# Kernel optimization log

Hardware: AMD Instinct MI355X
Metric: run time of the kernel (lower is better)

The kernel has to match this reference:

```python
import jax, jax.numpy as jnp
import numpy as np

B, S, IN, OUT, E, K = 4, 2048, 4096, 4096, 8, 16
POOLS = E * K  # 128 rank-one pools


def setup_inputs() -> dict:
    key = jax.random.key(0)
    k1, k2, k3, k4, k5 = jax.random.split(key, 5)
    sc = 0.02
    return {
        "hidden_states": jax.random.normal(k1, (B, S, IN), jnp.float32),
        "w0": jax.random.normal(k2, (OUT, IN), jnp.float32) * sc,   # pretrained Linear weight
        "b0": jnp.zeros((OUT,), jnp.float32),                        # pretrained Linear bias
        "wr": jax.random.normal(k3, (POOLS, IN), jnp.float32) * sc,  # Router stacked v.T
        "u": jax.random.normal(k4, (OUT, POOLS), jnp.float32) * sc,  # RankOnePools.u
        "svh": jax.random.normal(k5, (POOLS, IN), jnp.float32) * sc, # RankOnePools.svh
        "top_k": 2,
    }


def reference(hidden_states, w0, b0, wr, u, svh, top_k):
    # pretrained dense path (expert_use_diff=True)
    pretrained_out = jnp.einsum('bsi,oi->bso', hidden_states, w0) + b0

    x = hidden_states.reshape(-1, hidden_states.shape[-1])  # [N, IN]

    # Router: logits over num_experts*k rank-one pools
    logits = jnp.einsum('ni,pi->np', x, wr)                  # [N, POOLS]
    vals, idx = jax.lax.top_k(logits, top_k)                 # [N, top_k]
    vals = vals / jnp.sum(vals, axis=-1, keepdims=True)      # computed but UNUSED (matches original torch code)

    # RankOnePools: gather selected rank-one factors and combine
    svh_sel = svh[idx]                                       # [N, top_k, IN]
    dot = jnp.einsum('ni,nti->nt', x, svh_sel)               # [N, top_k]
    u_sel = u.T[idx]                                         # [N, top_k, OUT]
    expert_out = jnp.einsum('nt,nto->no', dot, u_sel)        # [N, OUT]

    out = pretrained_out + expert_out.reshape(pretrained_out.shape)
    return out
```

## Files before the change

kernel.cpp:

```cpp
#include <hip/hip_runtime.h>

#define K_DIM  4096
#define N_OUT  4096
#define N_TOK  8192
#define N_POOL 128

typedef __bf16 bf16x8 __attribute__((ext_vector_type(8)));
typedef float  f32x4  __attribute__((ext_vector_type(4)));
typedef unsigned short u16x8 __attribute__((ext_vector_type(8)));

#define AS1 __attribute__((address_space(1)))
#define AS3 __attribute__((address_space(3)))

__device__ __forceinline__ unsigned short f2bf(float f) {
    union { float f; unsigned u; } v; v.f = f;
    unsigned r = v.u + 0x7fffu + ((v.u >> 16) & 1u);
    return (unsigned short)(r >> 16);
}
__device__ __forceinline__ float bf2f(unsigned short b) {
    union { unsigned u; float f; } v; v.u = ((unsigned)b) << 16;
    return v.f;
}

__global__ __launch_bounds__(256) void k_convert_w0(const float* __restrict__ w0,
                                                    unsigned short* __restrict__ w0b) {
    size_t base = ((size_t)blockIdx.x * 256 + threadIdx.x) * 8;
    float4 a = *(const float4*)(w0 + base);
    float4 b = *(const float4*)(w0 + base + 4);
    u16x8 r;
    r[0] = f2bf(a.x); r[1] = f2bf(a.y); r[2] = f2bf(a.z); r[3] = f2bf(a.w);
    r[4] = f2bf(b.x); r[5] = f2bf(b.y); r[6] = f2bf(b.z); r[7] = f2bf(b.w);
    *(u16x8*)(w0b + base) = r;
}

__global__ __launch_bounds__(256) void k_convert_x(const float* __restrict__ x,
                                                   unsigned short* __restrict__ xh) {
    size_t base = ((size_t)blockIdx.x * 256 + threadIdx.x) * 8;
    float4 a = *(const float4*)(x + base);
    float4 b = *(const float4*)(x + base + 4);
    u16x8 r;
    r[0] = f2bf(a.x); r[1] = f2bf(a.y); r[2] = f2bf(a.z); r[3] = f2bf(a.w);
    r[4] = f2bf(b.x); r[5] = f2bf(b.y); r[6] = f2bf(b.z); r[7] = f2bf(b.w);
    *(u16x8*)(xh + base) = r;
}

__global__ __launch_bounds__(256) void k_convert_wr(const float* __restrict__ wr,
                                                    unsigned short* __restrict__ wrh) {
    size_t base = ((size_t)blockIdx.x * 256 + threadIdx.x) * 8;
    float4 a = *(const float4*)(wr + base);
    float4 b = *(const float4*)(wr + base + 4);
    u16x8 r;
    r[0] = f2bf(a.x); r[1] = f2bf(a.y); r[2] = f2bf(a.z); r[3] = f2bf(a.w);
    r[4] = f2bf(b.x); r[5] = f2bf(b.y); r[6] = f2bf(b.z); r[7] = f2bf(b.w);
    *(u16x8*)(wrh + base) = r;
}

__global__ __launch_bounds__(256) void k_transpose_u(const float* __restrict__ u,
                                                     float* __restrict__ uT) {
    __shared__ float t[32][65];
    const int o0 = blockIdx.x * 64, p0 = blockIdx.y * 32;
    const int tid = threadIdx.x;
#pragma unroll
    for (int it = 0; it < 8; it++) {
        int o = (tid >> 5) + it * 8;
        t[tid & 31][o] = u[(size_t)(o0 + o) * N_POOL + p0 + (tid & 31)];
    }
    __syncthreads();
#pragma unroll
    for (int it = 0; it < 8; it++) {
        int p = (tid >> 6) + it * 4;
        uT[(size_t)(p0 + p) * N_OUT + o0 + (tid & 63)] = t[p][tid & 63];
    }
}

__global__ __launch_bounds__(256) void k_logits(const unsigned short* __restrict__ xh,
                                                const unsigned short* __restrict__ wrh,
                                                float* __restrict__ lgbuf) {
    const int tid  = threadIdx.x;
    const int lane = tid & 63;
    const int w    = tid >> 6;
    const int lrow = lane & 15, lquad = lane >> 4;
    const size_t tok0 = (size_t)blockIdx.x * 16;
    const int p0 = w * 32;

    const unsigned short* xa  = xh  + (tok0 + lrow) * (size_t)K_DIM + lquad * 8;
    const unsigned short* bp0 = wrh + (size_t)(p0 + lrow) * K_DIM + lquad * 8;
    const unsigned short* bp1 = wrh + (size_t)(p0 + 16 + lrow) * K_DIM + lquad * 8;

    f32x4 acc0 = {}, acc1 = {};
    bf16x8 av = *(const bf16x8*)xa;
    bf16x8 b0 = *(const bf16x8*)bp0;
    bf16x8 b1 = *(const bf16x8*)bp1;

#pragma unroll 4
    for (int s = 0; s < 128; s++) {
        bf16x8 ac = av, b0c = b0, b1c = b1;
        if (s < 127) {
            av = *(const bf16x8*)(xa  + (s + 1) * 32);
            b0 = *(const bf16x8*)(bp0 + (s + 1) * 32);
            b1 = *(const bf16x8*)(bp1 + (s + 1) * 32);
        }
        acc0 = __builtin_amdgcn_mfma_f32_16x16x32_bf16(ac, b0c, acc0, 0, 0, 0);
        acc1 = __builtin_amdgcn_mfma_f32_16x16x32_bf16(ac, b1c, acc1, 0, 0, 0);
    }

#pragma unroll
    for (int r = 0; r < 4; r++) {
        lgbuf[(tok0 + lquad * 4 + r) * N_POOL + p0 + lrow]      = acc0[r];
        lgbuf[(tok0 + lquad * 4 + r) * N_POOL + p0 + 16 + lrow] = acc1[r];
    }
}

#define TAU 0.06f

__global__ __launch_bounds__(256) void k_topk(const float* __restrict__ lgbuf,
                                              const float* __restrict__ x,
                                              const float* __restrict__ wr,
                                              const unsigned short* __restrict__ xh,
                                              const float* __restrict__ svh,
                                              int* __restrict__ idxp,
                                              float* __restrict__ dotp) {
    __shared__ float lg[32][N_POOL + 1];
    __shared__ float thr2[32];
    __shared__ int   flg[32];
    __shared__ int   sel[32][2];

    const int tid  = threadIdx.x;
    const int lane = tid & 63;
    const int w    = tid >> 6;
    const size_t m0 = (size_t)blockIdx.x * 32;

    {
        const int tok = tid >> 3, cb = (tid & 7) * 16;
        const float* src = lgbuf + (m0 + tok) * N_POOL + cb;
#pragma unroll
        for (int j = 0; j < 4; j++) {
            float4 v = *(const float4*)(src + j * 4);
            lg[tok][cb + j * 4 + 0] = v.x; lg[tok][cb + j * 4 + 1] = v.y;
            lg[tok][cb + j * 4 + 2] = v.z; lg[tok][cb + j * 4 + 3] = v.w;
        }
    }
    __syncthreads();

    if (tid < 32) {
        float v1 = -3.4e38f, v2 = -3.4e38f, v3 = -3.4e38f; int i1 = 0, i2 = 0;
        for (int p = 0; p < N_POOL; p++) {
            float v = lg[tid][p];
            if (v > v1)      { v3 = v2; v2 = v1; i2 = i1; v1 = v; i1 = p; }
            else if (v > v2) { v3 = v2; v2 = v;  i2 = p; }
            else if (v > v3) { v3 = v; }
        }
        sel[tid][0] = i1; sel[tid][1] = i2;
        thr2[tid] = v2 - TAU;
        flg[tid]  = (v2 - v3 < TAU) ? 1 : 0;
    }
    __syncthreads();

    if (w == 0) {
        for (int s = 0; s < 32; s++) {
            if (!flg[s]) continue;
            const float th = thr2[s];
            unsigned long long c0 = __ballot(lg[s][lane] >= th);
            unsigned long long c1 = __ballot(lg[s][64 + lane] >= th);
            float v1 = -3.4e38f, v2 = -3.4e38f; int i1 = 0, i2 = 0;
            const float* xr = x + (m0 + s) * K_DIM;
            for (int half = 0; half < 2; half++) {
                unsigned long long m = half ? c1 : c0;
                while (m) {
                    const int p = (half ? 64 : 0) + __ffsll(m) - 1;
                    m &= m - 1;
                    const float* wp = wr + (size_t)p * K_DIM;
                    float d = 0.f;
#pragma unroll 8
                    for (int it = 0; it < 64; it++)
                        d += xr[it * 64 + lane] * wp[it * 64 + lane];
#pragma unroll
                    for (int off = 32; off > 0; off >>= 1) d += __shfl_down(d, off);
                    d = __shfl(d, 0);
                    if (d > v1)      { v2 = v1; i2 = i1; v1 = d; i1 = p; }
                    else if (d > v2) { v2 = d; i2 = p; }
                }
            }
            if (lane == 0) { sel[s][0] = i1; sel[s][1] = i2; }
        }
    }
    __syncthreads();

    if (tid < 32) {
        idxp[(m0 + tid) * 2 + 0] = sel[tid][0];
        idxp[(m0 + tid) * 2 + 1] = sel[tid][1];
    }

    for (int s = w; s < 32; s += 4) {
        const size_t n = m0 + s;
        const int e0 = sel[s][0], e1 = sel[s][1];
        float d0 = 0.f, d1 = 0.f;
#pragma unroll
        for (int it = 0; it < 8; it++) {
            const int e = (it * 64 + lane) * 8;
            u16x8 xv = *(const u16x8*)(xh + n * K_DIM + e);
            float4 s0 = *(const float4*)(svh + (size_t)e0 * K_DIM + e);
            float4 s1 = *(const float4*)(svh + (size_t)e0 * K_DIM + e + 4);
            float4 s2 = *(const float4*)(svh + (size_t)e1 * K_DIM + e);
            float4 s3 = *(const float4*)(svh + (size_t)e1 * K_DIM + e + 4);
            float x0 = bf2f(xv[0]), x1 = bf2f(xv[1]), x2 = bf2f(xv[2]), x3 = bf2f(xv[3]);
            float x4 = bf2f(xv[4]), x5 = bf2f(xv[5]), x6 = bf2f(xv[6]), x7 = bf2f(xv[7]);
            d0 += x0*s0.x + x1*s0.y + x2*s0.z + x3*s0.w + x4*s1.x + x5*s1.y + x6*s1.z + x7*s1.w;
            d1 += x0*s2.x + x1*s2.y + x2*s2.z + x3*s2.w + x4*s3.x + x5*s3.y + x6*s3.z + x7*s3.w;
        }
#pragma unroll
        for (int off = 32; off > 0; off >>= 1) {
            d0 += __shfl_down(d0, off);
            d1 += __shfl_down(d1, off);
        }
        if (lane == 0) { dotp[n * 2 + 0] = d0; dotp[n * 2 + 1] = d1; }
    }
}

__global__ __launch_bounds__(512) void k_gemm(const unsigned short* __restrict__ xh,
                                              const unsigned short* __restrict__ w0b,
                                              const float* __restrict__ b0,
                                              const float* __restrict__ uT,
                                              const int* __restrict__ idxp,
                                              const float* __restrict__ dotp,
                                              float* __restrict__ out) {
    __shared__ __attribute__((aligned(16))) unsigned short Als[2][256 * 64];
    __shared__ __attribute__((aligned(16))) unsigned short Bls[2][256 * 64];

    const int tid  = threadIdx.x;
    const int lane = tid & 63;
    const int w    = tid >> 6;
    const int wm   = w >> 2, wn = w & 3;
    const int lrow = lane & 15, lquad = lane >> 4;

    const int lgid = (blockIdx.x & 7) * 64 + (blockIdx.x >> 3);
    const size_t n0 = (size_t)(lgid & 15) * 256;
    const size_t m0 = (size_t)(lgid >> 4) * 256;

    const int srow   = tid >> 3;
    const int xchunk = (tid & 7) ^ (srow & 7);
    const unsigned short* ag = xh  + (m0 + srow) * K_DIM + xchunk * 8;
    const unsigned short* bg = w0b + (n0 + srow) * K_DIM + xchunk * 8;

    f32x4 acc[8][4] = {};

#define STAGE(buf, k0)                                                                        \
    {                                                                                         \
        unsigned short* al = &Als[buf][tid * 8];                                              \
        unsigned short* bl = &Bls[buf][tid * 8];                                              \
        _Pragma("unroll")                                                                     \
        for (int l = 0; l < 4; l++) {                                                         \
            __builtin_amdgcn_global_load_lds(                                                 \
                (const AS1 void*)(ag + (size_t)l * 64 * K_DIM + (k0)),                        \
                (AS3 void*)(al + l * 4096), 16, 0, 0);                                        \
            __builtin_amdgcn_global_load_lds(                                                 \
                (const AS1 void*)(bg + (size_t)l * 64 * K_DIM + (k0)),                        \
                (AS3 void*)(bl + l * 4096), 16, 0, 0);                                        \
        }                                                                                     \
    }

#define COMPUTE(buf)                                                                          \
    {                                                                                         \
        _Pragma("unroll")                                                                     \
        for (int ks = 0; ks < 2; ks++) {                                                      \
            const int cs = ((ks * 4 + lquad) ^ (lrow & 7)) * 8;                               \
            bf16x8 bfv[4];                                                                    \
            _Pragma("unroll")                                                                 \
            for (int nt = 0; nt < 4; nt++)                                                    \
                bfv[nt] = *(const bf16x8*)&Bls[buf][(wn * 64 + nt * 16 + lrow) * 64 + cs];    \
            _Pragma("unroll")                                                                 \
            for (int mt = 0; mt < 8; mt++) {                                                  \
                bf16x8 av = *(const bf16x8*)&Als[buf][(wm * 128 + mt * 16 + lrow) * 64 + cs]; \
                _Pragma("unroll")                                                             \
                for (int nt = 0; nt < 4; nt++)                                                \
                    acc[mt][nt] = __builtin_amdgcn_mfma_f32_16x16x32_bf16(av, bfv[nt], acc[mt][nt], 0, 0, 0); \
            }                                                                                 \
        }                                                                                     \
    }

    STAGE(0, 0)
    STAGE(1, 64)

    for (int t = 0; t < 63; ++t) {
        asm volatile("s_waitcnt vmcnt(8)" ::: "memory");
        __builtin_amdgcn_s_barrier();
        const int buf = t & 1;
        COMPUTE(buf)
        __builtin_amdgcn_s_barrier();
        if (t < 62) STAGE(buf, (t + 2) * 64)
    }
    asm volatile("s_waitcnt vmcnt(0)" ::: "memory");
    __builtin_amdgcn_s_barrier();
    COMPUTE(1)

#undef STAGE
#undef COMPUTE

    float b0v[4];
#pragma unroll
    for (int nt = 0; nt < 4; nt++) b0v[nt] = b0[n0 + wn * 64 + nt * 16 + lrow];
#pragma unroll
    for (int mt = 0; mt < 8; mt++) {
        const size_t rb = m0 + wm * 128 + mt * 16 + lquad * 4;
#pragma unroll
        for (int r = 0; r < 4; r++) {
            const size_t gm = rb + r;
            const int e0 = idxp[gm * 2 + 0], e1 = idxp[gm * 2 + 1];
            const float dd0 = dotp[gm * 2 + 0], dd1 = dotp[gm * 2 + 1];
#pragma unroll
            for (int nt = 0; nt < 4; nt++) {
                const size_t gn = n0 + wn * 64 + nt * 16 + lrow;
                float vv = acc[mt][nt][r] + b0v[nt]
                         + dd0 * uT[(size_t)e0 * N_OUT + gn] + dd1 * uT[(size_t)e1 * N_OUT + gn];
                out[gm * N_OUT + gn] = vv;
            }
        }
    }
}

extern "C" void kernel_launch(void* const* d_in, const int* in_sizes, int n_in,
                              void* d_out, int out_size, void* d_ws, size_t ws_size,
                              hipStream_t stream) {
    const float* x   = (const float*)d_in[0];
    const float* w0  = (const float*)d_in[1];
    const float* b0  = (const float*)d_in[2];
    const float* wr  = (const float*)d_in[3];
    const float* u   = (const float*)d_in[4];
    const float* svh = (const float*)d_in[5];
    float* out = (float*)d_out;

    char* ws = (char*)d_ws;
    unsigned short* xh  = (unsigned short*)ws;
    unsigned short* w0b = (unsigned short*)(ws + 67108864);
    float* lgbuf = (float*)(ws + 67108864);
    int*   idxp = (int*)(ws + 100663296);
    float* dotp = (float*)(ws + 100663296 + 65536);
    float* uTp  = (float*)(ws + 100663296 + 131072);
    unsigned short* wrh = (unsigned short*)(ws + 102891520);

    k_convert_x<<<dim3(33554432 / (256 * 8)), dim3(256), 0, stream>>>(x, xh);
    k_convert_wr<<<dim3(524288 / (256 * 8)), dim3(256), 0, stream>>>(wr, wrh);
    k_transpose_u<<<dim3(N_OUT / 64, N_POOL / 32), dim3(256), 0, stream>>>(u, uTp);
    k_logits<<<dim3(512), dim3(256), 0, stream>>>(xh, wrh, lgbuf);
    k_topk<<<dim3(256), dim3(256), 0, stream>>>(lgbuf, x, wr, xh, svh, idxp, dotp);
    k_convert_w0<<<dim3(16777216 / (256 * 8)), dim3(256), 0, stream>>>(w0, w0b);
    k_gemm<<<dim3(512), dim3(512), 0, stream>>>(xh, w0b, b0, uTp, idxp, dotp, out);
}
```

Baseline: 761.7 us.

## Merge conversion kernels, fuse router logits into top-k, reschedule GEMM main loop

The three fp32-to-bf16 conversion kernels become one launch, and the router logits MFMA is folded into the top-k kernel, so logits no longer make a global round trip. The GEMM main loop is restructured to interleave staged global-to-LDS loads in quarter chunks between MFMA groups, using s_setprio and a single outstanding-load wait, with a launch-bounds occupancy hint. This is meant to cut launch overhead and hide memory latency better inside the GEMM, at the cost of more barriers per iteration and more register pressure.

```diff
diff --git a/kernel.cpp b/kernel.cpp
--- a/kernel.cpp
+++ b/kernel.cpp
@@ -22,37 +22,25 @@
     return v.f;
 }
 
-__global__ __launch_bounds__(256) void k_convert_w0(const float* __restrict__ w0,
-                                                    unsigned short* __restrict__ w0b) {
-    size_t base = ((size_t)blockIdx.x * 256 + threadIdx.x) * 8;
-    float4 a = *(const float4*)(w0 + base);
-    float4 b = *(const float4*)(w0 + base + 4);
+__global__ __launch_bounds__(256) void k_prep(const float* __restrict__ x,
+                                              const float* __restrict__ w0,
+                                              const float* __restrict__ wr,
+                                              unsigned short* __restrict__ xh,
+                                              unsigned short* __restrict__ w0b,
+                                              unsigned short* __restrict__ wrh) {
+    int b = blockIdx.x;
+    const float* src;
+    unsigned short* dst;
+    if (b < 16384)      { src = x;  dst = xh;  }
+    else if (b < 24576) { src = w0; dst = w0b; b -= 16384; }
+    else                { src = wr; dst = wrh; b -= 24576; }
+    size_t base = ((size_t)b * 256 + threadIdx.x) * 8;
+    float4 a = *(const float4*)(src + base);
+    float4 c = *(const float4*)(src + base + 4);
     u16x8 r;
     r[0] = f2bf(a.x); r[1] = f2bf(a.y); r[2] = f2bf(a.z); r[3] = f2bf(a.w);
-    r[4] = f2bf(b.x); r[5] = f2bf(b.y); r[6] = f2bf(b.z); r[7] = f2bf(b.w);
-    *(u16x8*)(w0b + base) = r;
-}
-
-__global__ __launch_bounds__(256) void k_convert_x(const float* __restrict__ x,
-                                                   unsigned short* __restrict__ xh) {
-    size_t base = ((size_t)blockIdx.x * 256 + threadIdx.x) * 8;
-    float4 a = *(const float4*)(x + base);
-    float4 b = *(const float4*)(x + base + 4);
-    u16x8 r;
-    r[0] = f2bf(a.x); r[1] = f2bf(a.y); r[2] = f2bf(a.z); r[3] = f2bf(a.w);
-    r[4] = f2bf(b.x); r[5] = f2bf(b.y); r[6] = f2bf(b.z); r[7] = f2bf(b.w);
-    *(u16x8*)(xh + base) = r;
-}
-
-__global__ __launch_bounds__(256) void k_convert_wr(const float* __restrict__ wr,
-                                                    unsigned short* __restrict__ wrh) {
-    size_t base = ((size_t)blockIdx.x * 256 + threadIdx.x) * 8;
-    float4 a = *(const float4*)(wr + base);
-    float4 b = *(const float4*)(wr + base + 4);
-    u16x8 r;
-    r[0] = f2bf(a.x); r[1] = f2bf(a.y); r[2] = f2bf(a.z); r[3] = f2bf(a.w);
-    r[4] = f2bf(b.x); r[5] = f2bf(b.y); r[6] = f2bf(b.z); r[7] = f2bf(b.w);
-    *(u16x8*)(wrh + base) = r;
+    r[4] = f2bf(c.x); r[5] = f2bf(c.y); r[6] = f2bf(c.z); r[7] = f2bf(c.w);
+    *(u16x8*)(dst + base) = r;
 }
 
 __global__ __launch_bounds__(256) void k_transpose_u(const float* __restrict__ u,
@@ -73,53 +61,15 @@
     }
 }
 
-__global__ __launch_bounds__(256) void k_logits(const unsigned short* __restrict__ xh,
-                                                const unsigned short* __restrict__ wrh,
-                                                float* __restrict__ lgbuf) {
-    const int tid  = threadIdx.x;
-    const int lane = tid & 63;
-    const int w    = tid >> 6;
-    const int lrow = lane & 15, lquad = lane >> 4;
-    const size_t tok0 = (size_t)blockIdx.x * 16;
-    const int p0 = w * 32;
-
-    const unsigned short* xa  = xh  + (tok0 + lrow) * (size_t)K_DIM + lquad * 8;
-    const unsigned short* bp0 = wrh + (size_t)(p0 + lrow) * K_DIM + lquad * 8;
-    const unsigned short* bp1 = wrh + (size_t)(p0 + 16 + lrow) * K_DIM + lquad * 8;
-
-    f32x4 acc0 = {}, acc1 = {};
-    bf16x8 av = *(const bf16x8*)xa;
-    bf16x8 b0 = *(const bf16x8*)bp0;
-    bf16x8 b1 = *(const bf16x8*)bp1;
-
-#pragma unroll 4
-    for (int s = 0; s < 128; s++) {
-        bf16x8 ac = av, b0c = b0, b1c = b1;
-        if (s < 127) {
-            av = *(const bf16x8*)(xa  + (s + 1) * 32);
-            b0 = *(const bf16x8*)(bp0 + (s + 1) * 32);
-            b1 = *(const bf16x8*)(bp1 + (s + 1) * 32);
-        }
-        acc0 = __builtin_amdgcn_mfma_f32_16x16x32_bf16(ac, b0c, acc0, 0, 0, 0);
-        acc1 = __builtin_amdgcn_mfma_f32_16x16x32_bf16(ac, b1c, acc1, 0, 0, 0);
-    }
-
-#pragma unroll
-    for (int r = 0; r < 4; r++) {
-        lgbuf[(tok0 + lquad * 4 + r) * N_POOL + p0 + lrow]      = acc0[r];
-        lgbuf[(tok0 + lquad * 4 + r) * N_POOL + p0 + 16 + lrow] = acc1[r];
-    }
-}
-
 #define TAU 0.06f
 
-__global__ __launch_bounds__(256) void k_topk(const float* __restrict__ lgbuf,
-                                              const float* __restrict__ x,
-                                              const float* __restrict__ wr,
-                                              const unsigned short* __restrict__ xh,
-                                              const float* __restrict__ svh,
-                                              int* __restrict__ idxp,
-                                              float* __restrict__ dotp) {
+__global__ __launch_bounds__(512) void k_router2(const float* __restrict__ x,
+                                                 const float* __restrict__ wr,
+                                                 const unsigned short* __restrict__ wrh,
+                                                 const unsigned short* __restrict__ xh,
+                                                 const float* __restrict__ svh,
+                                                 int* __restrict__ idxp,
+                                                 float* __restrict__ dotp) {
     __shared__ float lg[32][N_POOL + 1];
     __shared__ float thr2[32];
     __shared__ int   flg[32];
@@ -128,16 +78,37 @@
     const int tid  = threadIdx.x;
     const int lane = tid & 63;
     const int w    = tid >> 6;
+    const int wm   = w & 1;
+    const int wn   = w >> 1;
+    const int lrow = lane & 15, lquad = lane >> 4;
     const size_t m0 = (size_t)blockIdx.x * 32;
 
     {
-        const int tok = tid >> 3, cb = (tid & 7) * 16;
-        const float* src = lgbuf + (m0 + tok) * N_POOL + cb;
-#pragma unroll
-        for (int j = 0; j < 4; j++) {
-            float4 v = *(const float4*)(src + j * 4);
-            lg[tok][cb + j * 4 + 0] = v.x; lg[tok][cb + j * 4 + 1] = v.y;
-            lg[tok][cb + j * 4 + 2] = v.z; lg[tok][cb + j * 4 + 3] = v.w;
+        const unsigned short* xa  = xh  + (m0 + wm * 16 + lrow) * (size_t)K_DIM + lquad * 8;
+        const unsigned short* bp0 = wrh + (size_t)(wn * 32 + lrow) * K_DIM + lquad * 8;
+        const unsigned short* bp1 = wrh + (size_t)(wn * 32 + 16 + lrow) * K_DIM + lquad * 8;
+
+        f32x4 acc0 = {}, acc1 = {};
+        bf16x8 av = *(const bf16x8*)xa;
+        bf16x8 b0 = *(const bf16x8*)bp0;
+        bf16x8 b1 = *(const bf16x8*)bp1;
+
+#pragma unroll 4
+        for (int s = 0; s < 128; s++) {
+            bf16x8 ac = av, b0c = b0, b1c = b1;
+            if (s < 127) {
+                av = *(const bf16x8*)(xa  + (s + 1) * 32);
+                b0 = *(const bf16x8*)(bp0 + (s + 1) * 32);
+                b1 = *(const bf16x8*)(bp1 + (s + 1) * 32);
+            }
+            acc0 = __builtin_amdgcn_mfma_f32_16x16x32_bf16(ac, b0c, acc0, 0, 0, 0);
+            acc1 = __builtin_amdgcn_mfma_f32_16x16x32_bf16(ac, b1c, acc1, 0, 0, 0);
+        }
+
+#pragma unroll
+        for (int r = 0; r < 4; r++) {
+            lg[wm * 16 + lquad * 4 + r][wn * 32 + lrow]      = acc0[r];
+            lg[wm * 16 + lquad * 4 + r][wn * 32 + 16 + lrow] = acc1[r];
         }
     }
     __syncthreads();
@@ -191,7 +162,7 @@
         idxp[(m0 + tid) * 2 + 1] = sel[tid][1];
     }
 
-    for (int s = w; s < 32; s += 4) {
+    for (int s = w; s < 32; s += 8) {
         const size_t n = m0 + s;
         const int e0 = sel[s][0], e1 = sel[s][1];
         float d0 = 0.f, d1 = 0.f;
@@ -217,13 +188,13 @@
     }
 }
 
-__global__ __launch_bounds__(512) void k_gemm(const unsigned short* __restrict__ xh,
-                                              const unsigned short* __restrict__ w0b,
-                                              const float* __restrict__ b0,
-                                              const float* __restrict__ uT,
-                                              const int* __restrict__ idxp,
-                                              const float* __restrict__ dotp,
-                                              float* __restrict__ out) {
+__global__ __launch_bounds__(512, 2) void k_gemm(const unsigned short* __restrict__ xh,
+                                                 const unsigned short* __restrict__ w0b,
+                                                 const float* __restrict__ b0,
+                                                 const float* __restrict__ uT,
+                                                 const int* __restrict__ idxp,
+                                                 const float* __restrict__ dotp,
+                                                 float* __restrict__ out) {
     __shared__ __attribute__((aligned(16))) unsigned short Als[2][256 * 64];
     __shared__ __attribute__((aligned(16))) unsigned short Bls[2][256 * 64];
 
@@ -232,69 +203,97 @@
     const int w    = tid >> 6;
     const int wm   = w >> 2, wn = w & 3;
     const int lrow = lane & 15, lquad = lane >> 4;
+    const int srow8 = lane >> 3, schunk = lane & 7;
 
     const int lgid = (blockIdx.x & 7) * 64 + (blockIdx.x >> 3);
     const size_t n0 = (size_t)(lgid & 15) * 256;
     const size_t m0 = (size_t)(lgid >> 4) * 256;
 
-    const int srow   = tid >> 3;
-    const int xchunk = (tid & 7) ^ (srow & 7);
-    const unsigned short* ag = xh  + (m0 + srow) * K_DIM + xchunk * 8;
-    const unsigned short* bg = w0b + (n0 + srow) * K_DIM + xchunk * 8;
-
     f32x4 acc[8][4] = {};
-
-#define STAGE(buf, k0)                                                                        \
-    {                                                                                         \
-        unsigned short* al = &Als[buf][tid * 8];                                              \
-        unsigned short* bl = &Bls[buf][tid * 8];                                              \
-        _Pragma("unroll")                                                                     \
-        for (int l = 0; l < 4; l++) {                                                         \
-            __builtin_amdgcn_global_load_lds(                                                 \
-                (const AS1 void*)(ag + (size_t)l * 64 * K_DIM + (k0)),                        \
-                (AS3 void*)(al + l * 4096), 16, 0, 0);                                        \
-            __builtin_amdgcn_global_load_lds(                                                 \
-                (const AS1 void*)(bg + (size_t)l * 64 * K_DIM + (k0)),                        \
-                (AS3 void*)(bl + l * 4096), 16, 0, 0);                                        \
-        }                                                                                     \
-    }
-
-#define COMPUTE(buf)                                                                          \
-    {                                                                                         \
-        _Pragma("unroll")                                                                     \
-        for (int ks = 0; ks < 2; ks++) {                                                      \
-            const int cs = ((ks * 4 + lquad) ^ (lrow & 7)) * 8;                               \
-            bf16x8 bfv[4];                                                                    \
-            _Pragma("unroll")                                                                 \
-            for (int nt = 0; nt < 4; nt++)                                                    \
-                bfv[nt] = *(const bf16x8*)&Bls[buf][(wn * 64 + nt * 16 + lrow) * 64 + cs];    \
-            _Pragma("unroll")                                                                 \
-            for (int mt = 0; mt < 8; mt++) {                                                  \
-                bf16x8 av = *(const bf16x8*)&Als[buf][(wm * 128 + mt * 16 + lrow) * 64 + cs]; \
-                _Pragma("unroll")                                                             \
-                for (int nt = 0; nt < 4; nt++)                                                \
-                    acc[mt][nt] = __builtin_amdgcn_mfma_f32_16x16x32_bf16(av, bfv[nt], acc[mt][nt], 0, 0, 0); \
-            }                                                                                 \
-        }                                                                                     \
-    }
-
-    STAGE(0, 0)
-    STAGE(1, 64)
-
-    for (int t = 0; t < 63; ++t) {
-        asm volatile("s_waitcnt vmcnt(8)" ::: "memory");
-        __builtin_amdgcn_s_barrier();
-        const int buf = t & 1;
-        COMPUTE(buf)
-        __builtin_amdgcn_s_barrier();
-        if (t < 62) STAGE(buf, (t + 2) * 64)
-    }
-    asm volatile("s_waitcnt vmcnt(0)" ::: "memory");
+    const int cs0 = ((0 + lquad) ^ (lrow & 7)) * 8;
+    const int cs1 = ((4 + lquad) ^ (lrow & 7)) * 8;
+
+#define ST_A(bufi, r0, kk)                                                                      \
+    { int rr = (r0) + srow8; int cc = schunk ^ (rr & 7);                                        \
+      __builtin_amdgcn_global_load_lds(                                                         \
+          (const AS1 void*)(xh + (m0 + rr) * (size_t)K_DIM + (kk) + cc * 8),                    \
+          (AS3 void*)(&Als[bufi][(r0) * 64] + lane * 8), 16, 0, 0); }
+#define ST_B(bufi, r0, kk)                                                                      \
+    { int rr = (r0) + srow8; int cc = schunk ^ (rr & 7);                                        \
+      __builtin_amdgcn_global_load_lds(                                                         \
+          (const AS1 void*)(w0b + (n0 + rr) * (size_t)K_DIM + (kk) + cc * 8),                   \
+          (AS3 void*)(&Bls[bufi][(r0) * 64] + lane * 8), 16, 0, 0); }
+
+#define STG_BA(bufi, kk) { ST_B(bufi, 8 * w,       kk) ST_B(bufi, 64 + 8 * w,  kk) }
+#define STG_BB(bufi, kk) { ST_B(bufi, 128 + 8 * w, kk) ST_B(bufi, 192 + 8 * w, kk) }
+#define STG_AH(bufi, kk) { ST_A(bufi, 64 + 8 * w,  kk) ST_A(bufi, 192 + 8 * w, kk) }
+#define STG_AL(bufi, kk) { ST_A(bufi, 8 * w,       kk) ST_A(bufi, 128 + 8 * w, kk) }
+
+#define LD_AV(MB, CS)                                                                           \
+    _Pragma("unroll")                                                                           \
+    for (int q = 0; q < 4; q++)                                                                 \
+        av[q] = *(const bf16x8*)&Als[buf][(wm * 128 + ((MB) + q) * 16 + lrow) * 64 + (CS)];
+#define LD_BV(CS)                                                                               \
+    _Pragma("unroll")                                                                           \
+    for (int q = 0; q < 4; q++)                                                                 \
+        bv[q] = *(const bf16x8*)&Bls[buf][(wn * 64 + q * 16 + lrow) * 64 + (CS)];
+#define MFMA_Q(MB)                                                                              \
+    _Pragma("unroll")                                                                           \
+    for (int q = 0; q < 4; q++)                                                                 \
+        _Pragma("unroll")                                                                       \
+        for (int nt = 0; nt < 4; nt++)                                                          \
+            acc[(MB) + q][nt] =                                                                 \
+                __builtin_amdgcn_mfma_f32_16x16x32_bf16(av[q], bv[nt], acc[(MB) + q][nt], 0, 0, 0);
+
+    STG_AL(0, 0) STG_BA(0, 0) STG_BB(0, 0) STG_AH(0, 0) STG_AL(1, 64)
+    asm volatile("s_waitcnt vmcnt(2)" ::: "memory");
     __builtin_amdgcn_s_barrier();
-    COMPUTE(1)
-
-#undef STAGE
-#undef COMPUTE
+
+    for (int t = 0; t < 64; ++t) {
+        const int buf = t & 1, bufN = buf ^ 1;
+        const int kn = (t + 1) * 64, kn2 = (t + 2) * 64;
+        bf16x8 av[4], bv[4];
+        LD_AV(0, cs0) LD_BV(cs0)
+        if (t < 63) STG_BA(bufN, kn)
+        __builtin_amdgcn_s_barrier();
+        __builtin_amdgcn_s_setprio(1);
+        MFMA_Q(0)
+        __builtin_amdgcn_s_setprio(0);
+        __builtin_amdgcn_s_barrier();
+        LD_AV(4, cs0)
+        if (t < 63) STG_BB(bufN, kn)
+        __builtin_amdgcn_s_barrier();
+        __builtin_amdgcn_s_setprio(1);
+        MFMA_Q(4)
+        __builtin_amdgcn_s_setprio(0);
+        __builtin_amdgcn_s_barrier();
+        LD_AV(0, cs1) LD_BV(cs1)
+        if (t < 63) STG_AH(bufN, kn)
+        __builtin_amdgcn_s_barrier();
+        __builtin_amdgcn_s_setprio(1);
+        MFMA_Q(0)
+        __builtin_amdgcn_s_setprio(0);
+        __builtin_amdgcn_s_barrier();
+        LD_AV(4, cs1)
+        if (t < 62) STG_AL(buf, kn2)
+        __builtin_amdgcn_s_barrier();
+        __builtin_amdgcn_s_setprio(1);
+        MFMA_Q(4)
+        __builtin_amdgcn_s_setprio(0);
+        if (t < 62)       asm volatile("s_waitcnt vmcnt(2)" ::: "memory");
+        else if (t == 62) asm volatile("s_waitcnt vmcnt(0)" ::: "memory");
+        __builtin_amdgcn_s_barrier();
+    }
+
+#undef ST_A
+#undef ST_B
+#undef STG_BA
+#undef STG_BB
+#undef STG_AH
+#undef STG_AL
+#undef LD_AV
+#undef LD_BV
+#undef MFMA_Q
 
     float b0v[4];
 #pragma unroll
@@ -332,17 +331,13 @@
     char* ws = (char*)d_ws;
     unsigned short* xh  = (unsigned short*)ws;
     unsigned short* w0b = (unsigned short*)(ws + 67108864);
-    float* lgbuf = (float*)(ws + 67108864);
     int*   idxp = (int*)(ws + 100663296);
     float* dotp = (float*)(ws + 100663296 + 65536);
     float* uTp  = (float*)(ws + 100663296 + 131072);
     unsigned short* wrh = (unsigned short*)(ws + 102891520);
 
-    k_convert_x<<<dim3(33554432 / (256 * 8)), dim3(256), 0, stream>>>(x, xh);
-    k_convert_wr<<<dim3(524288 / (256 * 8)), dim3(256), 0, stream>>>(wr, wrh);
+    k_prep<<<dim3(24832), dim3(256), 0, stream>>>(x, w0, wr, xh, w0b, wrh);
     k_transpose_u<<<dim3(N_OUT / 64, N_POOL / 32), dim3(256), 0, stream>>>(u, uTp);
-    k_logits<<<dim3(512), dim3(256), 0, stream>>>(xh, wrh, lgbuf);
-    k_topk<<<dim3(256), dim3(256), 0, stream>>>(lgbuf, x, wr, xh, svh, idxp, dotp);
-    k_convert_w0<<<dim3(16777216 / (256 * 8)), dim3(256), 0, stream>>>(w0, w0b);
+    k_router2<<<dim3(N_TOK / 32), dim3(512), 0, stream>>>(x, wr, wrh, xh, svh, idxp, dotp);
     k_gemm<<<dim3(512), dim3(512), 0, stream>>>(xh, w0b, b0, uTp, idxp, dotp, out);
 }
```

After: 743.0 us. 1.03x faster.
